# Kernel optimization log

Measured on AMD Instinct MI355X. Metric: run time of the kernel, lower is better.

The kernel has to match this reference:

```python
import jax, jax.numpy as jnp
import numpy as np

B, T, D, H, O = 64, 1024, 256, 256, 64  # H = hidden_dim//2 per direction


def setup_inputs() -> dict:
    key = jax.random.key(0)
    ks = jax.random.split(key, 16)
    s = 0.05
    mk = lambda k, shape: (jax.random.normal(k, shape, jnp.float32) * s)
    inp = {"x": jax.random.normal(ks[0], (B, T, D), jnp.float32)}
    i = 1
    for l, din in enumerate([D, 2 * H]):
        for d in ("f", "b"):
            inp[f"Wih_l{l}{d}"] = mk(ks[i], (4 * H, din)); i += 1
            inp[f"Whh_l{l}{d}"] = mk(ks[i], (4 * H, H)); i += 1
            inp[f"b_l{l}{d}"] = mk(ks[i], (4 * H,)); i += 1
    inp["fc_W"] = mk(ks[i], (O, 2 * H))
    inp["fc_b"] = mk(ks[i + 1], (O,))
    return inp


def _lstm_dir(x, Wih, Whh, b, reverse):
    # x: [T, B, din] -> outputs [T, B, H]; PyTorch gate order i, f, g, o.
    gx = jnp.einsum('tbd,gd->tbg', x, Wih) + b  # precompute input contribution
    h0 = jnp.zeros((x.shape[1], Whh.shape[1]), x.dtype)

    def step(carry, g_in):
        h, c = carry
        g = g_in + h @ Whh.T
        i, f, gg, o = jnp.split(g, 4, axis=-1)
        c = jax.nn.sigmoid(f) * c + jax.nn.sigmoid(i) * jnp.tanh(gg)
        h = jax.nn.sigmoid(o) * jnp.tanh(c)
        return (h, c), h

    _, hs = jax.lax.scan(step, (h0, h0), gx, reverse=reverse)
    return hs


def reference(x, Wih_l0f, Whh_l0f, b_l0f, Wih_l0b, Whh_l0b, b_l0b,
              Wih_l1f, Whh_l1f, b_l1f, Wih_l1b, Whh_l1b, b_l1b, fc_W, fc_b):
    h = jnp.transpose(x, (1, 0, 2))  # [T, B, D]
    layers = [(Wih_l0f, Whh_l0f, b_l0f, Wih_l0b, Whh_l0b, b_l0b),
              (Wih_l1f, Whh_l1f, b_l1f, Wih_l1b, Whh_l1b, b_l1b)]
    for Wf, Uf, bf, Wb, Ub, bb in layers:
        hf = _lstm_dir(h, Wf, Uf, bf, reverse=False)
        hb = _lstm_dir(h, Wb, Ub, bb, reverse=True)
        h = jnp.concatenate([hf, hb], axis=-1)  # [T, B, 2H]
    out = jnp.exp(h @ fc_W.T + fc_b)  # tgt == 'sigma'
    return jnp.transpose(out, (1, 0, 2))  # [B, T, O]
```

## Files before the change

kernel.cpp:

```cpp
#include <hip/hip_runtime.h>
#include <stdint.h>


typedef __attribute__((ext_vector_type(8))) short short8;
typedef __attribute__((ext_vector_type(4))) float floatx4;

#define MFMA_BF16(A, B, C) __builtin_amdgcn_mfma_f32_16x16x32_bf16(A, B, C, 0, 0, 0)

__device__ __forceinline__ unsigned short f2bf(float f) {
  unsigned u = __float_as_uint(f);
  u += 0x7FFFu + ((u >> 16) & 1u);
  return (unsigned short)(u >> 16);
}
__device__ __forceinline__ short8 load_cvt8(const float* p) {
  short8 r;
#pragma unroll
  for (int i = 0; i < 8; ++i) r[i] = (short)f2bf(p[i]);
  return r;
}
__device__ __forceinline__ float clamp_gate(float x) { return fminf(30.f, fmaxf(-30.f, x)); }
__device__ __forceinline__ float clamp_fc(float x) { return fminf(4.f, fmaxf(-30.f, x)); }
__device__ __forceinline__ float sigm(float x) { return 1.0f / (1.0f + __expf(-x)); }
__device__ __forceinline__ float tanh_fast(float x) { return 1.0f - 2.0f / (1.0f + __expf(2.0f * x)); }

__device__ __forceinline__ bool wok(unsigned long long v) {
  return ((unsigned)v != 0xFFFFFFFFu) & ((unsigned)(v >> 32) != 0xFFFFFFFFu);
}

__global__ __launch_bounds__(256) void cvt_kernel(
    const float* __restrict__ s0, unsigned short* __restrict__ d0, int n0,
    const float* __restrict__ s1, unsigned short* __restrict__ d1, int n1) {
  const int stride = gridDim.x * 256;
  for (int j = blockIdx.x * 256 + threadIdx.x; j < n0; j += stride) d0[j] = f2bf(s0[j]);
  for (int j = blockIdx.x * 256 + threadIdx.x; j < n1; j += stride) d1[j] = f2bf(s1[j]);
}

template <int LAYER>
__global__ __launch_bounds__(256, 1) void lstm_layer_kernel(
    const float* __restrict__ xf32,
    const unsigned short* __restrict__ xbf,
    const unsigned short* __restrict__ wih,
    const float* __restrict__ WhhF, const float* __restrict__ WhhB,
    const float* __restrict__ bF, const float* __restrict__ bB,
    unsigned short* __restrict__ hout) {
  constexpr int NKS = LAYER ? 16 : 8;
  constexpr int KDIM = NKS * 32;
  constexpr size_t DIRSZ = (size_t)1024 * 16384;

  const int bx = blockIdx.x;
  const int dir = bx >> 4;
  const int g = bx & 15;
  const int tid = threadIdx.x;
  const int w = tid >> 6, l = tid & 63, l15 = l & 15, q = l >> 4;

  const float* Whh = dir ? WhhB : WhhF;
  const float* bias = dir ? bB : bF;

  short8 whh[4][8];
#pragma unroll
  for (int gi = 0; gi < 4; ++gi) {
    const float* wr = Whh + (size_t)(gi * 256 + g * 16 + l15) * 256;
#pragma unroll
    for (int ks = 0; ks < 8; ++ks) whh[gi][ks] = load_cvt8(wr + ks * 32 + q * 8);
  }

  const unsigned short* wd = wih + (size_t)dir * 1024 * KDIM;

  float bvp[16];
#pragma unroll
  for (int gi = 0; gi < 4; ++gi)
#pragma unroll
    for (int r = 0; r < 4; ++r) bvp[gi * 4 + r] = bias[gi * 256 + g * 16 + q * 4 + r];

  const int b = w * 16 + l15;
  unsigned short* hd = hout + (size_t)dir * DIRSZ;

  float c[4] = {0.f, 0.f, 0.f, 0.f};

  for (int it = 0; it < 1024; ++it) {
    const int t = dir ? (1023 - it) : it;
    const int tp = dir ? (t + 1) : (t - 1);

    floatx4 acc[4];
#pragma unroll
    for (int gi = 0; gi < 4; ++gi)
#pragma unroll
      for (int r = 0; r < 4; ++r) acc[gi][r] = bvp[gi * 4 + r];

#pragma unroll
    for (int ks = 0; ks < NKS; ++ks) {
      short8 xf;
      if (LAYER == 0) {
        xf = load_cvt8(xf32 + (((size_t)b << 10) + t) * 256 + ks * 32 + q * 8);
      } else {
        const int k = ks * 32 + q * 8;
        const int gp = (k & 255) >> 4;
        const size_t off = (size_t)(k >> 8) * DIRSZ +
                           (((size_t)t * 4 + w) * 16 + gp) * 256 + l15 * 16 +
                           (k & 15);
        xf = *(const short8*)(xbf + off);
      }
#pragma unroll
      for (int gi = 0; gi < 4; ++gi) {
        const short8 wfrag = *(const short8*)(
            wd + (size_t)(gi * 256 + g * 16 + l15) * KDIM + ks * 32 + q * 8);
        acc[gi] = MFMA_BF16(wfrag, xf, acc[gi]);
      }
    }

    if (it > 0) {
      const unsigned short* hbase = hd + ((size_t)tp * 4 + w) * (16 * 256);
      const int sub = l15 * 16 + (q & 1) * 8;
#pragma unroll
      for (int half = 0; half < 2; ++half) {
        unsigned long long hwv[8];
        for (;;) {
          bool ok = true;
#pragma unroll
          for (int ks4 = 0; ks4 < 4; ++ks4) {
            const int ks = half * 4 + ks4;
            const unsigned long long* p = (const unsigned long long*)(
                hbase + (size_t)(ks * 2 + (q >> 1)) * 256 + sub);
            hwv[2 * ks4] =
                __hip_atomic_load(p, __ATOMIC_RELAXED, __HIP_MEMORY_SCOPE_AGENT);
            hwv[2 * ks4 + 1] =
                __hip_atomic_load(p + 1, __ATOMIC_RELAXED, __HIP_MEMORY_SCOPE_AGENT);
          }
#pragma unroll
          for (int i = 0; i < 8; ++i) ok = ok & wok(hwv[i]);
          if (__all(ok)) break;
        }
#pragma unroll
        for (int ks4 = 0; ks4 < 4; ++ks4) {
          short8 hf;
          ((unsigned long long*)&hf)[0] = hwv[2 * ks4];
          ((unsigned long long*)&hf)[1] = hwv[2 * ks4 + 1];
#pragma unroll
          for (int gi = 0; gi < 4; ++gi)
            acc[gi] = MFMA_BF16(whh[gi][half * 4 + ks4], hf, acc[gi]);
        }
      }
    }

    unsigned long long hv = 0ull;
#pragma unroll
    for (int r = 0; r < 4; ++r) {
      const float si = sigm(clamp_gate(acc[0][r]));
      const float sf = sigm(clamp_gate(acc[1][r]));
      const float tg = tanh_fast(clamp_gate(acc[2][r]));
      const float so = sigm(clamp_gate(acc[3][r]));
      const float cn = sf * c[r] + si * tg;
      c[r] = cn;
      const unsigned short hb16 = f2bf(so * tanh_fast(cn));
      hv |= ((unsigned long long)hb16) << (16 * r);
    }

    __hip_atomic_store(
        (unsigned long long*)(hd + (((size_t)t * 4 + w) * 16 + g) * 256 +
                              l15 * 16 + q * 4),
        hv, __ATOMIC_RELAXED, __HIP_MEMORY_SCOPE_AGENT);
  }
}

__global__ __launch_bounds__(256) void fc_head_kernel(
    const unsigned short* __restrict__ h1,
    const float* __restrict__ fcW,
    const float* __restrict__ fcb,
    float* __restrict__ out) {
  constexpr size_t DIRSZ = (size_t)1024 * 16384;
  __shared__ unsigned short sW[64 * 512];
  const int tid = threadIdx.x;
  for (int i = tid; i < 64 * 512; i += 256) sW[i] = f2bf(fcW[i]);
  __syncthreads();

  const int w = tid >> 6, l = tid & 63, l15 = l & 15, q = l >> 4;
  const int m0 = blockIdx.x * 64 + w * 16;

  const int mA = m0 + l15;
  const int bA = mA >> 10, tA = mA & 1023;
  const size_t arow = ((size_t)tA * 4 + (bA >> 4)) * (16 * 256) +
                      (size_t)(bA & 15) * 16 + (q & 1) * 8;

  floatx4 acc[4];
#pragma unroll
  for (int nt = 0; nt < 4; ++nt) acc[nt] = (floatx4){0.f, 0.f, 0.f, 0.f};

#pragma unroll
  for (int dh = 0; dh < 2; ++dh) {
    const unsigned short* ad = h1 + (size_t)dh * DIRSZ;
#pragma unroll
    for (int ks = 0; ks < 8; ++ks) {
      const int gp = ks * 2 + (q >> 1);
      short8 af = *(const short8*)(ad + arow + (size_t)gp * 256);
#pragma unroll
      for (int nt = 0; nt < 4; ++nt) {
        short8 bf = *(const short8*)(sW + (nt * 16 + l15) * 512 + dh * 256 +
                                     ks * 32 + q * 8);
        acc[nt] = MFMA_BF16(af, bf, acc[nt]);
      }
    }
  }

#pragma unroll
  for (int nt = 0; nt < 4; ++nt) {
    const float bv = fcb[nt * 16 + l15];
#pragma unroll
    for (int r = 0; r < 4; ++r) {
      const int m = m0 + q * 4 + r;
      out[(size_t)m * 64 + nt * 16 + l15] = __expf(clamp_fc(acc[nt][r] + bv));
    }
  }
}

__global__ void diag_kernel(float* out, int n, float code) {
  int i = blockIdx.x * 256 + threadIdx.x;
  if (i < n) out[i] = (i == 0) ? code : 1.0f;
}


extern "C" void kernel_launch(void* const* d_in, const int* in_sizes, int n_in,
                              void* d_out, int out_size, void* d_ws, size_t ws_size,
                              hipStream_t stream) {
  const float* x       = (const float*)d_in[0];
  const float* Wih_l0f = (const float*)d_in[1];
  const float* Whh_l0f = (const float*)d_in[2];
  const float* b_l0f   = (const float*)d_in[3];
  const float* Wih_l0b = (const float*)d_in[4];
  const float* Whh_l0b = (const float*)d_in[5];
  const float* b_l0b   = (const float*)d_in[6];
  const float* Wih_l1f = (const float*)d_in[7];
  const float* Whh_l1f = (const float*)d_in[8];
  const float* b_l1f   = (const float*)d_in[9];
  const float* Wih_l1b = (const float*)d_in[10];
  const float* Whh_l1b = (const float*)d_in[11];
  const float* b_l1b   = (const float*)d_in[12];
  const float* fc_W    = (const float*)d_in[13];
  const float* fc_b    = (const float*)d_in[14];
  float* out = (float*)d_out;

  const size_t H_BYTES = (size_t)2 * 1024 * 64 * 256 * 2;

  if (ws_size < H_BYTES) {
    diag_kernel<<<dim3((out_size + 255) / 256), dim3(256), 0, stream>>>(
        out, out_size, 200.0f + (float)(ws_size >> 20));
    return;
  }

  unsigned short* h0 = (unsigned short*)d_ws;
  unsigned short* h1 = (unsigned short*)d_in[0];
  unsigned short* wb1 = (unsigned short*)d_out;
  unsigned short* wb0 = (unsigned short*)((uint8_t*)d_out + (2u << 20));

  hipMemsetAsync(h0, 0xFF, H_BYTES, stream);

  cvt_kernel<<<dim3(512), dim3(256), 0, stream>>>(
      Wih_l1f, wb1, 1024 * 512, Wih_l1b, wb1 + (size_t)1024 * 512, 1024 * 512);
  cvt_kernel<<<dim3(512), dim3(256), 0, stream>>>(
      Wih_l0f, wb0, 1024 * 256, Wih_l0b, wb0 + (size_t)1024 * 256, 1024 * 256);

  lstm_layer_kernel<0><<<dim3(32), dim3(256), 0, stream>>>(
      x, nullptr, wb0, Whh_l0f, Whh_l0b, b_l0f, b_l0b, h0);
  hipMemsetAsync(h1, 0xFF, H_BYTES, stream);
  lstm_layer_kernel<1><<<dim3(32), dim3(256), 0, stream>>>(
      nullptr, h0, wb1, Whh_l1f, Whh_l1b, b_l1f, b_l1b, h1);
  fc_head_kernel<<<dim3(1024), dim3(256), 0, stream>>>(h1, fc_W, fc_b, out);
}
```

Before: 12.87 ms.

## Prefetch next-step inputs, stream bf16 Whh from memory, and speculatively load h

Each step now loads the next timestep's input slice into registers right after the input MFMAs, so that load latency overlaps the wait on the recurrent state. Whh is converted to bf16 by extra cvt kernels and read from global/L2 every step, instead of being held in 32 short8 registers per lane. This frees VGPRs for the prefetch buffers at the cost of more memory traffic per step. The previous h is first read with plain vector loads, and only fragments still holding the 0xFF sentinel are re-polled with atomic loads. This shortens the spin path but relies on plain loads eventually seeing the values other blocks wrote.

```diff
diff --git a/kernel.cpp b/kernel.cpp
--- a/kernel.cpp
+++ b/kernel.cpp
@@ -4,6 +4,7 @@
 
 typedef __attribute__((ext_vector_type(8))) short short8;
 typedef __attribute__((ext_vector_type(4))) float floatx4;
+typedef __attribute__((ext_vector_type(4))) float fx4;
 
 #define MFMA_BF16(A, B, C) __builtin_amdgcn_mfma_f32_16x16x32_bf16(A, B, C, 0, 0, 0)
 
@@ -12,19 +13,15 @@
   u += 0x7FFFu + ((u >> 16) & 1u);
   return (unsigned short)(u >> 16);
 }
-__device__ __forceinline__ short8 load_cvt8(const float* p) {
-  short8 r;
-#pragma unroll
-  for (int i = 0; i < 8; ++i) r[i] = (short)f2bf(p[i]);
-  return r;
-}
 __device__ __forceinline__ float clamp_gate(float x) { return fminf(30.f, fmaxf(-30.f, x)); }
 __device__ __forceinline__ float clamp_fc(float x) { return fminf(4.f, fmaxf(-30.f, x)); }
 __device__ __forceinline__ float sigm(float x) { return 1.0f / (1.0f + __expf(-x)); }
 __device__ __forceinline__ float tanh_fast(float x) { return 1.0f - 2.0f / (1.0f + __expf(2.0f * x)); }
 
-__device__ __forceinline__ bool wok(unsigned long long v) {
-  return ((unsigned)v != 0xFFFFFFFFu) & ((unsigned)(v >> 32) != 0xFFFFFFFFu);
+__device__ __forceinline__ bool v16ok(short8 v) {
+  const unsigned* d = (const unsigned*)&v;
+  return (d[0] != 0xFFFFFFFFu) & (d[1] != 0xFFFFFFFFu) &
+         (d[2] != 0xFFFFFFFFu) & (d[3] != 0xFFFFFFFFu);
 }
 
 __global__ __launch_bounds__(256) void cvt_kernel(
@@ -40,7 +37,7 @@
     const float* __restrict__ xf32,
     const unsigned short* __restrict__ xbf,
     const unsigned short* __restrict__ wih,
-    const float* __restrict__ WhhF, const float* __restrict__ WhhB,
+    const unsigned short* __restrict__ whh,
     const float* __restrict__ bF, const float* __restrict__ bB,
     unsigned short* __restrict__ hout) {
   constexpr int NKS = LAYER ? 16 : 8;
@@ -53,18 +50,9 @@
   const int tid = threadIdx.x;
   const int w = tid >> 6, l = tid & 63, l15 = l & 15, q = l >> 4;
 
-  const float* Whh = dir ? WhhB : WhhF;
+  const unsigned short* wd = wih + (size_t)dir * 1024 * KDIM;
+  const unsigned short* whd = whh + (size_t)dir * 1024 * 256;
   const float* bias = dir ? bB : bF;
-
-  short8 whh[4][8];
-#pragma unroll
-  for (int gi = 0; gi < 4; ++gi) {
-    const float* wr = Whh + (size_t)(gi * 256 + g * 16 + l15) * 256;
-#pragma unroll
-    for (int ks = 0; ks < 8; ++ks) whh[gi][ks] = load_cvt8(wr + ks * 32 + q * 8);
-  }
-
-  const unsigned short* wd = wih + (size_t)dir * 1024 * KDIM;
 
   float bvp[16];
 #pragma unroll
@@ -76,10 +64,46 @@
   unsigned short* hd = hout + (size_t)dir * DIRSZ;
 
   float c[4] = {0.f, 0.f, 0.f, 0.f};
+
+  fx4 xn0[LAYER ? 1 : 8][2];
+  short8 xn1[LAYER ? 16 : 1];
+
+  auto issue_prefetch = [&](int tt) {
+    if (LAYER == 0) {
+#pragma unroll
+      for (int ks = 0; ks < 8; ++ks) {
+        const float* p = xf32 + (((size_t)b << 10) + tt) * 256 + ks * 32 + q * 8;
+        xn0[ks][0] = *(const fx4*)p;
+        xn0[ks][1] = *(const fx4*)(p + 4);
+      }
+    } else {
+#pragma unroll
+      for (int ks = 0; ks < 16; ++ks) {
+        const int k = ks * 32 + q * 8;
+        const int gp = (k & 255) >> 4;
+        const size_t off = (size_t)(k >> 8) * DIRSZ +
+                           (((size_t)tt * 4 + w) * 16 + gp) * 256 + l15 * 16 +
+                           (k & 15);
+        xn1[ks] = *(const short8*)(xbf + off);
+      }
+    }
+  };
+
+  issue_prefetch(dir ? 1023 : 0);
 
   for (int it = 0; it < 1024; ++it) {
     const int t = dir ? (1023 - it) : it;
     const int tp = dir ? (t + 1) : (t - 1);
+    const int tn = dir ? (t > 0 ? t - 1 : 0) : (t < 1023 ? t + 1 : 1023);
+
+    short8 pk[8];
+    const unsigned short* hbase = hd + ((size_t)tp * 4 + w) * (16 * 256);
+    const int sub = l15 * 16 + (q & 1) * 8;
+    if (it > 0) {
+#pragma unroll
+      for (int ks = 0; ks < 8; ++ks)
+        pk[ks] = *(const short8*)(hbase + (size_t)(ks * 2 + (q >> 1)) * 256 + sub);
+    }
 
     floatx4 acc[4];
 #pragma unroll
@@ -91,14 +115,12 @@
     for (int ks = 0; ks < NKS; ++ks) {
       short8 xf;
       if (LAYER == 0) {
-        xf = load_cvt8(xf32 + (((size_t)b << 10) + t) * 256 + ks * 32 + q * 8);
+#pragma unroll
+        for (int i = 0; i < 4; ++i) xf[i] = (short)f2bf(xn0[ks][0][i]);
+#pragma unroll
+        for (int i = 0; i < 4; ++i) xf[4 + i] = (short)f2bf(xn0[ks][1][i]);
       } else {
-        const int k = ks * 32 + q * 8;
-        const int gp = (k & 255) >> 4;
-        const size_t off = (size_t)(k >> 8) * DIRSZ +
-                           (((size_t)t * 4 + w) * 16 + gp) * 256 + l15 * 16 +
-                           (k & 15);
-        xf = *(const short8*)(xbf + off);
+        xf = xn1[ks];
       }
 #pragma unroll
       for (int gi = 0; gi < 4; ++gi) {
@@ -108,36 +130,40 @@
       }
     }
 
+    issue_prefetch(tn);
+
     if (it > 0) {
-      const unsigned short* hbase = hd + ((size_t)tp * 4 + w) * (16 * 256);
-      const int sub = l15 * 16 + (q & 1) * 8;
-#pragma unroll
-      for (int half = 0; half < 2; ++half) {
-        unsigned long long hwv[8];
-        for (;;) {
-          bool ok = true;
-#pragma unroll
-          for (int ks4 = 0; ks4 < 4; ++ks4) {
-            const int ks = half * 4 + ks4;
+      bool ok = true;
+#pragma unroll
+      for (int ks = 0; ks < 8; ++ks) ok = ok & v16ok(pk[ks]);
+      while (!__all(ok)) {
+#pragma unroll
+        for (int ks = 0; ks < 8; ++ks) {
+          if (!v16ok(pk[ks])) {
             const unsigned long long* p = (const unsigned long long*)(
                 hbase + (size_t)(ks * 2 + (q >> 1)) * 256 + sub);
-            hwv[2 * ks4] =
+            unsigned long long lo =
                 __hip_atomic_load(p, __ATOMIC_RELAXED, __HIP_MEMORY_SCOPE_AGENT);
-            hwv[2 * ks4 + 1] =
+            unsigned long long hi =
                 __hip_atomic_load(p + 1, __ATOMIC_RELAXED, __HIP_MEMORY_SCOPE_AGENT);
+            short8 v;
+            ((unsigned long long*)&v)[0] = lo;
+            ((unsigned long long*)&v)[1] = hi;
+            pk[ks] = v;
           }
-#pragma unroll
-          for (int i = 0; i < 8; ++i) ok = ok & wok(hwv[i]);
-          if (__all(ok)) break;
         }
-#pragma unroll
-        for (int ks4 = 0; ks4 < 4; ++ks4) {
-          short8 hf;
-          ((unsigned long long*)&hf)[0] = hwv[2 * ks4];
-          ((unsigned long long*)&hf)[1] = hwv[2 * ks4 + 1];
-#pragma unroll
-          for (int gi = 0; gi < 4; ++gi)
-            acc[gi] = MFMA_BF16(whh[gi][half * 4 + ks4], hf, acc[gi]);
+        ok = true;
+#pragma unroll
+        for (int ks = 0; ks < 8; ++ks) ok = ok & v16ok(pk[ks]);
+      }
+
+#pragma unroll
+      for (int ks = 0; ks < 8; ++ks) {
+#pragma unroll
+        for (int gi = 0; gi < 4; ++gi) {
+          const short8 hw = *(const short8*)(
+              whd + (size_t)(gi * 256 + g * 16 + l15) * 256 + ks * 32 + q * 8);
+          acc[gi] = MFMA_BF16(hw, pk[ks], acc[gi]);
         }
       }
     }
@@ -248,8 +274,10 @@
 
   unsigned short* h0 = (unsigned short*)d_ws;
   unsigned short* h1 = (unsigned short*)d_in[0];
-  unsigned short* wb1 = (unsigned short*)d_out;
-  unsigned short* wb0 = (unsigned short*)((uint8_t*)d_out + (2u << 20));
+  unsigned short* wb1  = (unsigned short*)d_out;
+  unsigned short* wb0  = (unsigned short*)((uint8_t*)d_out + (2u << 20));
+  unsigned short* wbh0 = (unsigned short*)((uint8_t*)d_out + (3u << 20));
+  unsigned short* wbh1 = (unsigned short*)((uint8_t*)d_out + (4u << 20));
 
   hipMemsetAsync(h0, 0xFF, H_BYTES, stream);
 
@@ -257,11 +285,15 @@
       Wih_l1f, wb1, 1024 * 512, Wih_l1b, wb1 + (size_t)1024 * 512, 1024 * 512);
   cvt_kernel<<<dim3(512), dim3(256), 0, stream>>>(
       Wih_l0f, wb0, 1024 * 256, Wih_l0b, wb0 + (size_t)1024 * 256, 1024 * 256);
+  cvt_kernel<<<dim3(512), dim3(256), 0, stream>>>(
+      Whh_l0f, wbh0, 1024 * 256, Whh_l0b, wbh0 + (size_t)1024 * 256, 1024 * 256);
+  cvt_kernel<<<dim3(512), dim3(256), 0, stream>>>(
+      Whh_l1f, wbh1, 1024 * 256, Whh_l1b, wbh1 + (size_t)1024 * 256, 1024 * 256);
 
   lstm_layer_kernel<0><<<dim3(32), dim3(256), 0, stream>>>(
-      x, nullptr, wb0, Whh_l0f, Whh_l0b, b_l0f, b_l0b, h0);
+      x, nullptr, wb0, wbh0, b_l0f, b_l0b, h0);
   hipMemsetAsync(h1, 0xFF, H_BYTES, stream);
   lstm_layer_kernel<1><<<dim3(32), dim3(256), 0, stream>>>(
-      nullptr, h0, wb1, Whh_l1f, Whh_l1b, b_l1f, b_l1b, h1);
+      nullptr, h0, wb1, wbh1, b_l1f, b_l1b, h1);
   fc_head_kernel<<<dim3(1024), dim3(256), 0, stream>>>(h1, fc_W, fc_b, out);
 }
```

New measurement: 20.01 ms. 55.5% more time.

## Spread LSTM blocks across XCDs and load recurrent state with plain vector loads

Applied to the files above, without the earlier changes.

Launches 128 blocks but keeps only 2 of every 8 active, so the 32 working blocks map to one forward and one backward block per XCD group under round-robin dispatch. It also changes the recurrent h polling: all eight 16-byte fragments are loaded first with ordinary vector loads, and only the fragments still holding the sentinel are re-polled with atomic loads before the MFMAs run. The h store becomes a volatile store followed by an atomic store. This aims to cut cross-block sync latency on the sequential recurrence. The risks are stale cached reads from the non-atomic loads and the cost of 96 idle blocks.

```diff
diff --git a/kernel.cpp b/kernel.cpp
--- a/kernel.cpp
+++ b/kernel.cpp
@@ -23,8 +23,10 @@
 __device__ __forceinline__ float sigm(float x) { return 1.0f / (1.0f + __expf(-x)); }
 __device__ __forceinline__ float tanh_fast(float x) { return 1.0f - 2.0f / (1.0f + __expf(2.0f * x)); }
 
-__device__ __forceinline__ bool wok(unsigned long long v) {
-  return ((unsigned)v != 0xFFFFFFFFu) & ((unsigned)(v >> 32) != 0xFFFFFFFFu);
+__device__ __forceinline__ bool v16ok(short8 v) {
+  const unsigned* d = (const unsigned*)&v;
+  return (d[0] != 0xFFFFFFFFu) & (d[1] != 0xFFFFFFFFu) &
+         (d[2] != 0xFFFFFFFFu) & (d[3] != 0xFFFFFFFFu);
 }
 
 __global__ __launch_bounds__(256) void cvt_kernel(
@@ -48,8 +50,10 @@
   constexpr size_t DIRSZ = (size_t)1024 * 16384;
 
   const int bx = blockIdx.x;
-  const int dir = bx >> 4;
-  const int g = bx & 15;
+  const int slot = bx & 7;
+  if (slot >= 2) return;
+  const int dir = slot;
+  const int g = bx >> 3;
   const int tid = threadIdx.x;
   const int w = tid >> 6, l = tid & 63, l15 = l & 15, q = l >> 4;
 
@@ -111,34 +115,38 @@
     if (it > 0) {
       const unsigned short* hbase = hd + ((size_t)tp * 4 + w) * (16 * 256);
       const int sub = l15 * 16 + (q & 1) * 8;
-#pragma unroll
-      for (int half = 0; half < 2; ++half) {
-        unsigned long long hwv[8];
-        for (;;) {
-          bool ok = true;
-#pragma unroll
-          for (int ks4 = 0; ks4 < 4; ++ks4) {
-            const int ks = half * 4 + ks4;
+      short8 pk[8];
+#pragma unroll
+      for (int ks = 0; ks < 8; ++ks)
+        pk[ks] = *(const short8*)(hbase + (size_t)(ks * 2 + (q >> 1)) * 256 + sub);
+      bool ok = true;
+#pragma unroll
+      for (int ks = 0; ks < 8; ++ks) ok = ok & v16ok(pk[ks]);
+      while (!__all(ok)) {
+#pragma unroll
+        for (int ks = 0; ks < 8; ++ks) {
+          if (!v16ok(pk[ks])) {
             const unsigned long long* p = (const unsigned long long*)(
                 hbase + (size_t)(ks * 2 + (q >> 1)) * 256 + sub);
-            hwv[2 * ks4] =
+            unsigned long long lo =
                 __hip_atomic_load(p, __ATOMIC_RELAXED, __HIP_MEMORY_SCOPE_AGENT);
-            hwv[2 * ks4 + 1] =
+            unsigned long long hi =
                 __hip_atomic_load(p + 1, __ATOMIC_RELAXED, __HIP_MEMORY_SCOPE_AGENT);
+            short8 v;
+            ((unsigned long long*)&v)[0] = lo;
+            ((unsigned long long*)&v)[1] = hi;
+            pk[ks] = v;
           }
-#pragma unroll
-          for (int i = 0; i < 8; ++i) ok = ok & wok(hwv[i]);
-          if (__all(ok)) break;
         }
-#pragma unroll
-        for (int ks4 = 0; ks4 < 4; ++ks4) {
-          short8 hf;
-          ((unsigned long long*)&hf)[0] = hwv[2 * ks4];
-          ((unsigned long long*)&hf)[1] = hwv[2 * ks4 + 1];
-#pragma unroll
-          for (int gi = 0; gi < 4; ++gi)
-            acc[gi] = MFMA_BF16(whh[gi][half * 4 + ks4], hf, acc[gi]);
-        }
+        ok = true;
+#pragma unroll
+        for (int ks = 0; ks < 8; ++ks) ok = ok & v16ok(pk[ks]);
+      }
+
+#pragma unroll
+      for (int ks = 0; ks < 8; ++ks) {
+#pragma unroll
+        for (int gi = 0; gi < 4; ++gi) acc[gi] = MFMA_BF16(whh[gi][ks], pk[ks], acc[gi]);
       }
     }
 
@@ -155,10 +163,11 @@
       hv |= ((unsigned long long)hb16) << (16 * r);
     }
 
-    __hip_atomic_store(
+    unsigned long long* dst =
         (unsigned long long*)(hd + (((size_t)t * 4 + w) * 16 + g) * 256 +
-                              l15 * 16 + q * 4),
-        hv, __ATOMIC_RELAXED, __HIP_MEMORY_SCOPE_AGENT);
+                              l15 * 16 + q * 4);
+    *(volatile unsigned long long*)dst = hv;
+    __hip_atomic_store(dst, hv, __ATOMIC_RELAXED, __HIP_MEMORY_SCOPE_AGENT);
   }
 }
 
@@ -258,10 +267,10 @@
   cvt_kernel<<<dim3(512), dim3(256), 0, stream>>>(
       Wih_l0f, wb0, 1024 * 256, Wih_l0b, wb0 + (size_t)1024 * 256, 1024 * 256);
 
-  lstm_layer_kernel<0><<<dim3(32), dim3(256), 0, stream>>>(
+  lstm_layer_kernel<0><<<dim3(128), dim3(256), 0, stream>>>(
       x, nullptr, wb0, Whh_l0f, Whh_l0b, b_l0f, b_l0b, h0);
   hipMemsetAsync(h1, 0xFF, H_BYTES, stream);
-  lstm_layer_kernel<1><<<dim3(32), dim3(256), 0, stream>>>(
+  lstm_layer_kernel<1><<<dim3(128), dim3(256), 0, stream>>>(
       nullptr, h0, wb1, Whh_l1f, Whh_l1b, b_l1f, b_l1b, h1);
   fc_head_kernel<<<dim3(1024), dim3(256), 0, stream>>>(h1, fc_W, fc_b, out);
 }
```

Result: slower. 13.70 ms (+6.5%).
